# Kernel optimization log

Measured on AMD Instinct MI355X. Metric: run time of the kernel, lower is better.

## Reference

```python
import jax, jax.numpy as jnp
import numpy as np

D_MODEL = 1024
NHEAD = 16
D_HEAD = D_MODEL // NHEAD


def setup_inputs() -> dict:
    key = jax.random.key(0)
    ks = jax.random.split(key, 9)
    B, S = 2, 2048
    scale = 1.0 / np.sqrt(D_MODEL)
    x = jax.random.normal(ks[0], (B, S, D_MODEL), dtype=jnp.float32)
    Wq = jax.random.normal(ks[1], (D_MODEL, D_MODEL), dtype=jnp.float32) * scale
    Wk = jax.random.normal(ks[2], (D_MODEL, D_MODEL), dtype=jnp.float32) * scale
    Wv = jax.random.normal(ks[3], (D_MODEL, D_MODEL), dtype=jnp.float32) * scale
    Wo = jax.random.normal(ks[4], (D_MODEL, D_MODEL), dtype=jnp.float32) * scale
    bq = jax.random.normal(ks[5], (D_MODEL,), dtype=jnp.float32) * 0.01
    bk = jax.random.normal(ks[6], (D_MODEL,), dtype=jnp.float32) * 0.01
    bv = jax.random.normal(ks[7], (D_MODEL,), dtype=jnp.float32) * 0.01
    bo = jax.random.normal(ks[8], (D_MODEL,), dtype=jnp.float32) * 0.01
    return {"x": x, "Wq": Wq, "bq": bq, "Wk": Wk, "bk": bk,
            "Wv": Wv, "bv": bv, "Wo": Wo, "bo": bo}


def reference(x, Wq, bq, Wk, bk, Wv, bv, Wo, bo):
    B, S, D = x.shape
    H, Dh = NHEAD, D_HEAD
    # projections; weights stored as (in, out) so y = x @ W + b
    def split_heads(t):  # [B,S,D] -> [B,H,S,Dh]
        return t.reshape(B, S, H, Dh).transpose(0, 2, 1, 3)
    q = split_heads(x @ Wq + bq)
    k = split_heads(x @ Wk + bk)
    v = split_heads(x @ Wv + bv)
    scale = 1.0 / jnp.sqrt(jnp.asarray(Dh, dtype=x.dtype))
    attn = jnp.einsum("bhqd,bhkd->bhqk", q, k) * scale  # [B,H,S,S]
    attn = jax.nn.softmax(attn, axis=-1)
    out = jnp.einsum("bhqk,bhkd->bhqd", attn, v)  # [B,H,S,Dh]
    out = out.transpose(0, 2, 1, 3).reshape(B, S, D)
    return out @ Wo + bo
```

## Files before the change

kernel.cpp:

```cpp
#include <hip/hip_runtime.h>
#include <hip/hip_bf16.h>
#include <stdint.h>
#include <stddef.h>

typedef __bf16 b16;
typedef __bf16 b16x4 __attribute__((ext_vector_type(4)));
typedef __bf16 b16x8 __attribute__((ext_vector_type(8)));
typedef float  f32x4 __attribute__((ext_vector_type(4)));

#define LOG2E 1.4426950408889634f
#define QSCALE (0.125f * LOG2E)

#if __has_builtin(__builtin_amdgcn_exp2f)
#define EXP2F(x) __builtin_amdgcn_exp2f(x)
#else
#define EXP2F(x) exp2f(x)
#endif

typedef __attribute__((address_space(1))) void gvoid;
typedef __attribute__((address_space(3))) void svoid;

__device__ __forceinline__ void async_cp16(void* lds, const void* g) {
    __builtin_amdgcn_global_load_lds((gvoid*)(void*)g, (svoid*)lds, 16, 0, 0);
}

#define SW(r) ((((r) & 7)) ^ (((r) >> 1) & 4))

__global__ __launch_bounds__(256) void k_prep(const float* __restrict__ x,
                                              const float* __restrict__ Wq,
                                              const float* __restrict__ Wk,
                                              const float* __restrict__ Wv,
                                              const float* __restrict__ Wo,
                                              b16* __restrict__ Xb,
                                              b16* __restrict__ WtQKV,
                                              b16* __restrict__ Wot) {
    const int z = blockIdx.z;
    if (z == 4) {
        const int blk = blockIdx.y * 32 + blockIdx.x;
        const float* src = x + (size_t)blk * 4096;
        b16* dst = Xb + (size_t)blk * 4096;
#pragma unroll
        for (int c = 0; c < 4; ++c) {
            const int i = c * 1024 + threadIdx.x * 4;
            float4 v = *(const float4*)(src + i);
            b16x4 o = { (b16)v.x, (b16)v.y, (b16)v.z, (b16)v.w };
            *(b16x4*)(dst + i) = o;
        }
        return;
    }
    __shared__ float t[32][33];
    const float* W = (z == 0) ? Wq : (z == 1) ? Wk : (z == 2) ? Wv : Wo;
    const int k0 = blockIdx.x * 32, n0 = blockIdx.y * 32;
    const int tr = threadIdx.x >> 3, tc4 = (threadIdx.x & 7) * 4;
    float4 v = *(const float4*)(W + (size_t)(k0 + tr) * 1024 + n0 + tc4);
    t[tr][tc4 + 0] = v.x; t[tr][tc4 + 1] = v.y;
    t[tr][tc4 + 2] = v.z; t[tr][tc4 + 3] = v.w;
    __syncthreads();
    b16* dst = (z < 3) ? (WtQKV + ((size_t)z << 20)) : Wot;
    b16x4 o = { (b16)t[tc4 + 0][tr], (b16)t[tc4 + 1][tr],
                (b16)t[tc4 + 2][tr], (b16)t[tc4 + 3][tr] };
    *(b16x4*)(dst + (size_t)(n0 + tr) * 1024 + k0 + tc4) = o;
}

__device__ __forceinline__ void gemm128_core(const b16* __restrict__ Ag,
                                             const b16* __restrict__ Bg,
                                             b16* As, b16* Bs, int tid,
                                             f32x4 acc[4][4]) {
    const int lane = tid & 63, wave = tid >> 6;
    const int wm = wave & 1, wn = wave >> 1;
    const int quad = lane >> 4, lc = lane & 15;
    const int ci0 = tid, ci1 = tid + 256;
    const b16* a0 = Ag + (ci0 >> 2) * 1024 + (ci0 & 3) * 8;
    const b16* a1 = Ag + (ci1 >> 2) * 1024 + (ci1 & 3) * 8;
    const b16* b0 = Bg + (ci0 >> 2) * 1024 + (ci0 & 3) * 8;
    const b16* b1 = Bg + (ci1 >> 2) * 1024 + (ci1 & 3) * 8;

#define GSTAGE(BUF, K0) do {                                   \
        async_cp16(As + (BUF) * 4096 + ci0 * 8, a0 + (K0));    \
        async_cp16(As + (BUF) * 4096 + ci1 * 8, a1 + (K0));    \
        async_cp16(Bs + (BUF) * 4096 + ci0 * 8, b0 + (K0));    \
        async_cp16(Bs + (BUF) * 4096 + ci1 * 8, b1 + (K0));    \
    } while (0)

#define GSTEP(BUF, SBUF, SK0, VM, DOSTAGE) do {                          \
        if (DOSTAGE) GSTAGE(SBUF, SK0);                                  \
        asm volatile("s_waitcnt vmcnt(" #VM ")" ::: "memory");           \
        __builtin_amdgcn_s_barrier();                                    \
        __builtin_amdgcn_sched_barrier(0);                               \
        b16x8 af[4], bfr[4];                                             \
        const b16* Al = As + (BUF) * 4096;                               \
        const b16* Bl = Bs + (BUF) * 4096;                               \
        _Pragma("unroll")                                                \
        for (int mt = 0; mt < 4; ++mt)                                   \
            af[mt] = *(const b16x8*)(Al + (wm * 64 + mt * 16 + lc) * 32 + quad * 8); \
        _Pragma("unroll")                                                \
        for (int nt = 0; nt < 4; ++nt)                                   \
            bfr[nt] = *(const b16x8*)(Bl + (wn * 64 + nt * 16 + lc) * 32 + quad * 8); \
        asm volatile("s_waitcnt lgkmcnt(0)" ::: "memory");               \
        __builtin_amdgcn_sched_barrier(0);                               \
        __builtin_amdgcn_s_barrier();                                    \
        __builtin_amdgcn_s_setprio(1);                                   \
        _Pragma("unroll")                                                \
        for (int mt = 0; mt < 4; ++mt)                                   \
            _Pragma("unroll")                                            \
            for (int nt = 0; nt < 4; ++nt)                               \
                acc[mt][nt] = __builtin_amdgcn_mfma_f32_16x16x32_bf16(   \
                    af[mt], bfr[nt], acc[mt][nt], 0, 0, 0);              \
        __builtin_amdgcn_s_setprio(0);                                   \
    } while (0)

    GSTAGE(0, 0);
    GSTAGE(1, 32);
    for (int i = 0; i < 10; ++i) {
        const int kb = 96 * i;
        GSTEP(0, 2, kb + 64, 8, 1);
        GSTEP(1, 0, kb + 96, 8, 1);
        GSTEP(2, 1, kb + 128, 8, 1);
    }
    GSTEP(0, 0, 0, 4, 0);
    GSTEP(1, 0, 0, 0, 0);
#undef GSTEP
#undef GSTAGE
}

__global__ __launch_bounds__(256, 3) void k_gemm_qkv(
    const b16* __restrict__ A, const b16* __restrict__ Bt,
    const float* __restrict__ bq, const float* __restrict__ bk,
    const float* __restrict__ bv,
    b16* __restrict__ Qg, b16* __restrict__ Kg, b16* __restrict__ Vtg) {
    __shared__ __align__(16) b16 LB[24576];
    b16* As = LB;
    b16* Bs = LB + 12288;
    char* Tb = (char*)LB;
    const int bm = blockIdx.x, bn = blockIdx.y;
    const int tid = threadIdx.x;
    const int lane = tid & 63, wave = tid >> 6;
    const int wm = wave & 1, wn = wave >> 1;
    const int quad = lane >> 4, lc = lane & 15;

    f32x4 acc[4][4] = {};
    gemm128_core(A + (size_t)(bm * 128) * 1024, Bt + (size_t)(bn * 128) * 1024,
                 As, Bs, tid, acc);

    const int mat = bn >> 3;
    const float* bp = (mat == 0) ? bq : (mat == 1) ? bk : bv;
    const float scl = (mat == 0) ? QSCALE : 1.0f;

#pragma unroll
    for (int nt = 0; nt < 4; ++nt) {
        const int ln = wn * 64 + nt * 16 + lc;
        const float bval = bp[(bn * 128 + ln) & 1023];
#pragma unroll
        for (int mt = 0; mt < 4; ++mt) {
            const int lm = wm * 64 + mt * 16 + quad * 4;
            if (mat == 2) {
                b16x4 o;
#pragma unroll
                for (int r = 0; r < 4; ++r) o[r] = (b16)(acc[mt][nt][r] + bval);
                const int byte = ln * 256 + (((lm >> 3) ^ (ln & 15)) << 4) + (lm & 7) * 2;
                *(b16x4*)(Tb + byte) = o;
            } else {
#pragma unroll
                for (int r = 0; r < 4; ++r) {
                    const int row = lm + r;
                    const int byte = row * 256 + (((ln >> 3) ^ (row & 15)) << 4) + (ln & 7) * 2;
                    *(b16*)(Tb + byte) = (b16)((acc[mt][nt][r] + bval) * scl);
                }
            }
        }
    }
    __syncthreads();

    const int chunk = tid & 7, hr0 = tid >> 3;
    const int b = bm >> 4;
    const int s_blk = (bm * 128) & 2047;
#pragma unroll
    for (int p = 0; p < 8; ++p) {
        const int hr = p * 32 + hr0;
        const int row = hr >> 1, half = hr & 1;
        const int c2 = (half * 8 + chunk) ^ (row & 15);
        b16x8 v = *(const b16x8*)(Tb + row * 256 + c2 * 16);
        if (mat == 2) {
            const int cm = (bn * 128 + row) & 1023;
            const int h = cm >> 6, dh = cm & 63;
            *(b16x8*)(Vtg + (size_t)((b * 16 + h) * 64 + dh) * 2048 +
                      s_blk + half * 64 + chunk * 8) = v;
        } else {
            const int s = s_blk + row;
            const int cm = (bn * 128 + half * 64 + chunk * 8) & 1023;
            const int h = cm >> 6, dh = cm & 63;
            b16* dst = (mat == 0) ? Qg : Kg;
            *(b16x8*)(dst + ((size_t)(b * 16 + h) * 2048 + s) * 64 + dh) = v;
        }
    }
}

__global__ __launch_bounds__(256, 2) void k_flash(
    const b16* __restrict__ Qg, const b16* __restrict__ Kg,
    const b16* __restrict__ Vtg,
    float* __restrict__ Opart, float* __restrict__ lpart,
    b16* __restrict__ AO, int ktiles, int direct, int np) {
    __shared__ __align__(16) b16 Ks[2 * 64 * 64];
    __shared__ __align__(16) b16 Vs[2 * 64 * 64];
    __shared__ float Lred[4][64];

    const int bid = blockIdx.x;
    const int gstride = np << 5;
    const int qb = bid / gstride;
    const int rem = bid - qb * gstride;
    const int bh = rem / np;
    const int part = rem - bh * np;

    const int tid = threadIdx.x, lane = tid & 63, wave = tid >> 6;
    const int quad = lane >> 4, lc = lane & 15;

    const b16* Kbh = Kg + (size_t)bh * 2048 * 64;
    const b16* Vbh = Vtg + (size_t)bh * 64 * 2048;
    const int kt0 = part * ktiles;

    const int ci0 = tid, ci1 = tid + 256;
    const int r0 = ci0 >> 3, gc0 = (ci0 & 7) ^ SW(r0);
    const int r1 = ci1 >> 3, gc1 = (ci1 & 7) ^ SW(r1);
    const b16* pK0 = Kbh + (size_t)(kt0 * 64 + r0) * 64 + gc0 * 8;
    const b16* pK1 = Kbh + (size_t)(kt0 * 64 + r1) * 64 + gc1 * 8;
    const b16* pV0 = Vbh + (size_t)r0 * 2048 + kt0 * 64 + gc0 * 8;
    const b16* pV1 = Vbh + (size_t)r1 * 2048 + kt0 * 64 + gc1 * 8;

#define FSTAGE(BUF) do {                                   \
        async_cp16(Ks + (BUF) * 4096 + ci0 * 8, pK0);      \
        async_cp16(Ks + (BUF) * 4096 + ci1 * 8, pK1);      \
        async_cp16(Vs + (BUF) * 4096 + ci0 * 8, pV0);      \
        async_cp16(Vs + (BUF) * 4096 + ci1 * 8, pV1);      \
        pK0 += 4096; pK1 += 4096; pV0 += 64; pV1 += 64;    \
    } while (0)

    FSTAGE(0);

    const b16* Qbase = Qg + ((size_t)bh * 2048 + qb * 256 + wave * 64) * 64;
    b16x8 qf[4][2];
#pragma unroll
    for (int qt = 0; qt < 4; ++qt)
#pragma unroll
        for (int ch = 0; ch < 2; ++ch)
            qf[qt][ch] = *(const b16x8*)(Qbase + (qt * 16 + lc) * 64 + ch * 32 + quad * 8);

    f32x4 oacc[4][4] = {};
    float lsum[4] = {0.f, 0.f, 0.f, 0.f};

    auto flash_tile = [&](const b16* Kc, const b16* Vc) {
#pragma unroll
        for (int ks = 0; ks < 2; ++ks) {
            b16x8 pf[4];
#pragma unroll
            for (int t = 0; t < 2; ++t) {
                const int krow = ks * 32 + (lc >> 2) * 8 + t * 4 + (lc & 3);
                b16x8 kf0 = *(const b16x8*)(Kc + krow * 64 + ((0 * 4 + quad) ^ SW(krow)) * 8);
                b16x8 kf1 = *(const b16x8*)(Kc + krow * 64 + ((1 * 4 + quad) ^ SW(krow)) * 8);
#pragma unroll
                for (int qt = 0; qt < 4; ++qt) {
                    f32x4 s = {};
                    s = __builtin_amdgcn_mfma_f32_16x16x32_bf16(kf0, qf[qt][0], s, 0, 0, 0);
                    s = __builtin_amdgcn_mfma_f32_16x16x32_bf16(kf1, qf[qt][1], s, 0, 0, 0);
                    float e0 = EXP2F(s[0]), e1 = EXP2F(s[1]);
                    float e2 = EXP2F(s[2]), e3 = EXP2F(s[3]);
                    lsum[qt] += (e0 + e1) + (e2 + e3);
                    pf[qt][t * 4 + 0] = (b16)e0;
                    pf[qt][t * 4 + 1] = (b16)e1;
                    pf[qt][t * 4 + 2] = (b16)e2;
                    pf[qt][t * 4 + 3] = (b16)e3;
                }
            }
            b16x8 vf[4];
#pragma unroll
            for (int dt = 0; dt < 4; ++dt) {
                const int row = dt * 16 + lc;
                vf[dt] = *(const b16x8*)(Vc + row * 64 + ((ks * 4 + quad) ^ SW(row)) * 8);
            }
            __builtin_amdgcn_s_setprio(1);
#pragma unroll
            for (int qt = 0; qt < 4; ++qt)
#pragma unroll
                for (int dt = 0; dt < 4; ++dt)
                    oacc[qt][dt] = __builtin_amdgcn_mfma_f32_16x16x32_bf16(
                        pf[qt], vf[dt], oacc[qt][dt], 0, 0, 0);
            __builtin_amdgcn_s_setprio(0);
        }
    };

    for (int kt = 0; kt < ktiles; kt += 2) {
        FSTAGE(1);
        asm volatile("s_waitcnt vmcnt(4)" ::: "memory");
        __builtin_amdgcn_s_barrier();
        __builtin_amdgcn_sched_barrier(0);
        flash_tile(Ks, Vs);
        __builtin_amdgcn_sched_barrier(0);
        __builtin_amdgcn_s_barrier();
        if (kt + 2 < ktiles) {
            FSTAGE(0);
            asm volatile("s_waitcnt vmcnt(4)" ::: "memory");
        } else {
            asm volatile("s_waitcnt vmcnt(0)" ::: "memory");
        }
        __builtin_amdgcn_s_barrier();
        __builtin_amdgcn_sched_barrier(0);
        flash_tile(Ks + 4096, Vs + 4096);
        __builtin_amdgcn_sched_barrier(0);
        __builtin_amdgcn_s_barrier();
    }
#undef FSTAGE

#pragma unroll
    for (int qt = 0; qt < 4; ++qt) {
        lsum[qt] += __shfl_xor(lsum[qt], 16, 64);
        lsum[qt] += __shfl_xor(lsum[qt], 32, 64);
    }

    if (!direct) {
        float* Op = Opart + ((size_t)(part * 32 + bh) * 2048 + qb * 256 + wave * 64) * 64;
#pragma unroll
        for (int qt = 0; qt < 4; ++qt)
#pragma unroll
            for (int dt = 0; dt < 4; ++dt)
#pragma unroll
                for (int r = 0; r < 4; ++r)
                    Op[(qt * 16 + quad * 4 + r) * 64 + dt * 16 + lc] = oacc[qt][dt][r];
        if (quad == 0) {
            float* lp = lpart + (size_t)(part * 32 + bh) * 2048 + qb * 256 + wave * 64;
#pragma unroll
            for (int qt = 0; qt < 4; ++qt) lp[qt * 16 + lc] = lsum[qt];
        }
    } else {
        if (quad == 0) {
#pragma unroll
            for (int qt = 0; qt < 4; ++qt) Lred[wave][qt * 16 + lc] = lsum[qt];
        }
        const int b = bh >> 4, h = bh & 15;
#pragma unroll
        for (int qt = 0; qt < 4; ++qt)
#pragma unroll
            for (int r = 0; r < 4; ++r) {
                const float inv = 1.0f / Lred[wave][qt * 16 + quad * 4 + r];
                const int s = qb * 256 + wave * 64 + qt * 16 + quad * 4 + r;
#pragma unroll
                for (int dt = 0; dt < 4; ++dt)
                    AO[(size_t)(b * 2048 + s) * 1024 + h * 64 + dt * 16 + lc] =
                        (b16)(oacc[qt][dt][r] * inv);
            }
    }
}

__global__ __launch_bounds__(256) void k_merge(const float* __restrict__ Opart,
                                               const float* __restrict__ lpart,
                                               b16* __restrict__ AO, int np) {
    const int bh = blockIdx.y;
    const int q = blockIdx.x * 16 + (threadIdx.x >> 4);
    const int d4 = (threadIdx.x & 15) * 4;
    const size_t qi = (size_t)bh * 2048 + q;
    f32x4 o = *(const f32x4*)(Opart + qi * 64 + d4);
    float l = lpart[qi];
    if (np == 2) {
        o += *(const f32x4*)(Opart + (qi + (size_t)32 * 2048) * 64 + d4);
        l += lpart[qi + (size_t)32 * 2048];
    }
    const float inv = 1.0f / l;
    const int b = bh >> 4, h = bh & 15;
    b16x4 ob = { (b16)(o[0] * inv), (b16)(o[1] * inv),
                 (b16)(o[2] * inv), (b16)(o[3] * inv) };
    *(b16x4*)(AO + (size_t)(b * 2048 + q) * 1024 + h * 64 + d4) = ob;
}

__global__ __launch_bounds__(256, 3) void k_gemm_out(
    const b16* __restrict__ A, const b16* __restrict__ Bt,
    const float* __restrict__ bo, float* __restrict__ out) {
    __shared__ __align__(16) b16 As[3 * 128 * 32];
    __shared__ __align__(16) b16 Bs[3 * 128 * 32];
    const int bm = blockIdx.x, bn = blockIdx.y;
    const int tid = threadIdx.x;
    const int lane = tid & 63, wave = tid >> 6;
    const int wm = wave & 1, wn = wave >> 1;
    const int quad = lane >> 4, lc = lane & 15;

    f32x4 acc[4][4] = {};
    gemm128_core(A + (size_t)(bm * 128) * 1024, Bt + (size_t)(bn * 128) * 1024,
                 As, Bs, tid, acc);

#pragma unroll
    for (int nt = 0; nt < 4; ++nt) {
        const int n = bn * 128 + wn * 64 + nt * 16 + lc;
        const float bval = bo[n];
#pragma unroll
        for (int mt = 0; mt < 4; ++mt) {
            const int m0 = bm * 128 + wm * 64 + mt * 16 + quad * 4;
#pragma unroll
            for (int r = 0; r < 4; ++r)
                out[(size_t)(m0 + r) * 1024 + n] = acc[mt][nt][r] + bval;
        }
    }
}

extern "C" void kernel_launch(void* const* d_in, const int* in_sizes, int n_in,
                              void* d_out, int out_size, void* d_ws, size_t ws_size,
                              hipStream_t stream) {
    const float* x  = (const float*)d_in[0];
    const float* Wq = (const float*)d_in[1];
    const float* bq = (const float*)d_in[2];
    const float* Wk = (const float*)d_in[3];
    const float* bk = (const float*)d_in[4];
    const float* Wv = (const float*)d_in[5];
    const float* bv = (const float*)d_in[6];
    const float* Wo = (const float*)d_in[7];
    const float* bo = (const float*)d_in[8];
    float* out = (float*)d_out;

    char* ws = (char*)d_ws;
    const size_t MB = 1024 * 1024;
    b16* Xb  = (b16*)(ws);
    b16* AO  = (b16*)(ws);
    b16* WtQ = (b16*)(ws + 8 * MB);
    b16* Wot = (b16*)(ws + 14 * MB);
    b16* Qg  = (b16*)(ws + 16 * MB);
    b16* Kg  = (b16*)(ws + 24 * MB);
    b16* Vtg = (b16*)(ws + 32 * MB);

    const size_t need2 = 40 * MB + 2 * (16 * MB) + 2 * 256 * 1024;
    const int np = (ws_size >= need2) ? 2 : 1;
    float* Opart = (float*)(ws + 40 * MB);
    float* lpart = (float*)(ws + 40 * MB + (size_t)np * 16 * MB);
    const int direct = (np == 1);

    k_prep<<<dim3(32, 32, 5), 256, 0, stream>>>(x, Wq, Wk, Wv, Wo, Xb, WtQ, Wot);
    k_gemm_qkv<<<dim3(32, 24), 256, 0, stream>>>(Xb, WtQ, bq, bk, bv, Qg, Kg, Vtg);
    k_flash<<<dim3(8 * 32 * np), 256, 0, stream>>>(Qg, Kg, Vtg, Opart, lpart, AO,
                                                   32 / np, direct, np);
    if (!direct)
        k_merge<<<dim3(128, 32), 256, 0, stream>>>(Opart, lpart, AO, np);
    k_gemm_out<<<dim3(32, 8), 256, 0, stream>>>(AO, Wot, bo, out);
}
```

Before: 189.3 us.

## Triple-buffer K/V tiles in flash attention and drop trailing barrier

The flash attention kernel moves from double to triple buffering of the K and V tiles in LDS. Buffer pointers rotate after each tile, and the prologue prefetches two tiles ahead. Each iteration now needs only one barrier, because the buffer being refilled was last read a full iteration earlier. The aim is deeper load/compute overlap and less synchronisation, at the cost of more LDS per block, which could limit how many blocks fit on a CU.

After: 191.0 us. Within noise of the previous version (+0.9%).

```diff
diff --git a/kernel.cpp b/kernel.cpp
--- a/kernel.cpp
+++ b/kernel.cpp
@@ -200,8 +200,8 @@
     const b16* __restrict__ Vtg,
     float* __restrict__ Opart, float* __restrict__ lpart,
     b16* __restrict__ AO, int ktiles, int direct, int np) {
-    __shared__ __align__(16) b16 Ks[2 * 64 * 64];
-    __shared__ __align__(16) b16 Vs[2 * 64 * 64];
+    __shared__ __align__(16) b16 Ks[3 * 64 * 64];
+    __shared__ __align__(16) b16 Vs[3 * 64 * 64];
     __shared__ float Lred[4][64];
 
     const int bid = blockIdx.x;
@@ -226,15 +226,20 @@
     const b16* pV0 = Vbh + (size_t)r0 * 2048 + kt0 * 64 + gc0 * 8;
     const b16* pV1 = Vbh + (size_t)r1 * 2048 + kt0 * 64 + gc1 * 8;
 
-#define FSTAGE(BUF) do {                                   \
-        async_cp16(Ks + (BUF) * 4096 + ci0 * 8, pK0);      \
-        async_cp16(Ks + (BUF) * 4096 + ci1 * 8, pK1);      \
-        async_cp16(Vs + (BUF) * 4096 + ci0 * 8, pV0);      \
-        async_cp16(Vs + (BUF) * 4096 + ci1 * 8, pV1);      \
-        pK0 += 4096; pK1 += 4096; pV0 += 64; pV1 += 64;    \
+#define FSTAGE(KD, VD) do {                          \
+        async_cp16((KD) + ci0 * 8, pK0);             \
+        async_cp16((KD) + ci1 * 8, pK1);             \
+        async_cp16((VD) + ci0 * 8, pV0);             \
+        async_cp16((VD) + ci1 * 8, pV1);             \
+        pK0 += 4096; pK1 += 4096; pV0 += 64; pV1 += 64; \
     } while (0)
 
-    FSTAGE(0);
+    b16 *ka = Ks, *kb = Ks + 4096, *kc = Ks + 8192;
+    b16 *va = Vs, *vb = Vs + 4096, *vc = Vs + 8192;
+
+    FSTAGE(ka, va);
+    FSTAGE(kb, vb);
+    __builtin_amdgcn_sched_barrier(0);
 
     const b16* Qbase = Qg + ((size_t)bh * 2048 + qb * 256 + wave * 64) * 64;
     b16x8 qf[4][2];
@@ -287,25 +292,28 @@
         }
     };
 
-    for (int kt = 0; kt < ktiles; kt += 2) {
-        FSTAGE(1);
-        asm volatile("s_waitcnt vmcnt(4)" ::: "memory");
-        __builtin_amdgcn_s_barrier();
-        __builtin_amdgcn_sched_barrier(0);
-        flash_tile(Ks, Vs);
-        __builtin_amdgcn_sched_barrier(0);
-        __builtin_amdgcn_s_barrier();
-        if (kt + 2 < ktiles) {
-            FSTAGE(0);
+    asm volatile("s_waitcnt vmcnt(12)" ::: "memory");
+    __builtin_amdgcn_s_barrier();
+    __builtin_amdgcn_sched_barrier(0);
+    FSTAGE(kc, vc);
+    flash_tile(ka, va);
+    __builtin_amdgcn_sched_barrier(0);
+    { b16* t0 = ka; ka = kb; kb = kc; kc = t0;
+      b16* t1 = va; va = vb; vb = vc; vc = t1; }
+
+    for (int t = 1; t < ktiles; ++t) {
+        if (t < ktiles - 1) {
             asm volatile("s_waitcnt vmcnt(4)" ::: "memory");
         } else {
             asm volatile("s_waitcnt vmcnt(0)" ::: "memory");
         }
         __builtin_amdgcn_s_barrier();
         __builtin_amdgcn_sched_barrier(0);
-        flash_tile(Ks + 4096, Vs + 4096);
+        if (t + 2 < ktiles) FSTAGE(kc, vc);
+        flash_tile(ka, va);
         __builtin_amdgcn_sched_barrier(0);
-        __builtin_amdgcn_s_barrier();
+        b16* t0 = ka; ka = kb; kb = kc; kc = t0;
+        b16* t1 = va; va = vb; vb = vc; vc = t1;
     }
 #undef FSTAGE
 
```
